# Performance work log

Measured on AMD Instinct MI355X. Metric: run time of the kernel, lower is better.

The kernel has to match this reference:

```python
import jax, jax.numpy as jnp
import numpy as np

E = 1024
H = 16
DH = E // H
LN_EPS = 1e-5


def setup_inputs() -> dict:
    key = jax.random.key(0)
    ks = jax.random.split(key, 9)
    B, Lq, Lk = 8, 1024, 1024
    s = 0.02
    return {
        "query": jax.random.normal(ks[0], (B, Lq, E), jnp.float32),
        "key_t": jax.random.normal(ks[1], (B, Lk, E), jnp.float32),
        "value": jax.random.normal(ks[2], (B, Lk, E), jnp.float32),
        "in_proj_w": jax.random.normal(ks[3], (3 * E, E), jnp.float32) * s,
        "in_proj_b": jnp.zeros((3 * E,), jnp.float32),
        "out_proj_w": jax.random.normal(ks[4], (E, E), jnp.float32) * s,
        "out_proj_b": jnp.zeros((E,), jnp.float32),
        "ln_gamma": jnp.ones((E,), jnp.float32),
        "ln_beta": jnp.zeros((E,), jnp.float32),
    }


def _mha_cross(query, key_t, value, in_proj_w, in_proj_b, out_proj_w, out_proj_b,
               ln_gamma, ln_beta):
    B, Lq, _ = query.shape
    Lk = key_t.shape[1]
    wq, wk, wv = in_proj_w[:E], in_proj_w[E:2 * E], in_proj_w[2 * E:]
    bq, bk, bv = in_proj_b[:E], in_proj_b[E:2 * E], in_proj_b[2 * E:]
    # projections (torch Linear: x @ W^T + b)
    q = (query @ wq.T + bq).reshape(B, Lq, H, DH)
    k = (key_t @ wk.T + bk).reshape(B, Lk, H, DH)
    v = (value @ wv.T + bv).reshape(B, Lk, H, DH)
    scale = 1.0 / np.sqrt(DH).astype(np.float32)
    # unfused attention: explicit [B,H,Lq,Lk] scores (need_weights=True path)
    scores = jnp.einsum("bqhd,bkhd->bhqk", q, k) * scale
    probs = jax.nn.softmax(scores, axis=-1)
    attn = jnp.einsum("bhqk,bkhd->bqhd", probs, v).reshape(B, Lq, E)
    attn_out = attn @ out_proj_w.T + out_proj_b
    # averaged attention weights (average_attn_weights=True default)
    attn_weights = probs.mean(axis=1)  # [B, Lq, Lk]
    # residual + LayerNorm
    x = query + attn_out
    mu = x.mean(axis=-1, keepdims=True)
    var = x.var(axis=-1, keepdims=True)
    y = (x - mu) * jax.lax.rsqrt(var + LN_EPS) * ln_gamma + ln_beta
    return y, attn_weights


def reference(query, key_t, value, in_proj_w, in_proj_b, out_proj_w, out_proj_b,
              ln_gamma, ln_beta):
    return _mha_cross(query, key_t, value, in_proj_w, in_proj_b,
                      out_proj_w, out_proj_b, ln_gamma, ln_beta)
```

## Files before the change

### kernel.cpp

```cpp
#include <hip/hip_runtime.h>
#include <stdint.h>

#define E_DIM 1024
#define H_NUM 16
#define B_NUM 8
#define LQ 1024
#define LK 1024
#define MROWS (B_NUM * LQ)

typedef unsigned short u16;
typedef __attribute__((ext_vector_type(8))) short bf16x8;
typedef __attribute__((ext_vector_type(4))) short bf16x4;
typedef __attribute__((ext_vector_type(4))) float f32x4;
typedef __attribute__((ext_vector_type(2))) unsigned int u32x2;
typedef bf16x8 __attribute__((may_alias)) bf16x8_ma;
typedef bf16x4 __attribute__((may_alias)) bf16x4_ma;
typedef f32x4 __attribute__((may_alias)) f32x4_ma;
typedef u32x2 __attribute__((may_alias)) u32x2_ma;

typedef __attribute__((address_space(1))) const void* gas_ptr;
typedef __attribute__((address_space(3))) void* las_ptr;

__device__ __forceinline__ void gload16(const void* g, void* l) {
  __builtin_amdgcn_global_load_lds((gas_ptr)g, (las_ptr)l, 16, 0, 0);
}

__device__ __forceinline__ u16 f2bf(float f) {
  union { float f; uint32_t u; } c; c.f = f;
  return (u16)((c.u + 0x7FFFu + ((c.u >> 16) & 1u)) >> 16);
}

__device__ __forceinline__ uint32_t pack2bf(float lo, float hi) {
  return __builtin_amdgcn_perm(__float_as_uint(hi), __float_as_uint(lo), 0x07060302u);
}

#define MFMA_BF16(a, b, c) __builtin_amdgcn_mfma_f32_16x16x32_bf16((a), (b), (c), 0, 0, 0)

#define SCALE_Q 0.18033688011112042f


__global__ __launch_bounds__(256) void cvt_f32_bf16(const float* __restrict__ src,
                                                    u16* __restrict__ dst, int n4) {
  int i = blockIdx.x * 256 + threadIdx.x;
  const int stride = gridDim.x * 256;
  for (; i < n4; i += stride) {
    float4 v = ((const float4*)src)[i];
    ushort4 o;
    o.x = f2bf(v.x); o.y = f2bf(v.y); o.z = f2bf(v.z); o.w = f2bf(v.w);
    ((ushort4*)dst)[i] = o;
  }
}

__global__ __launch_bounds__(256) void cvt3_f32_bf16(
    const float* __restrict__ a0, const float* __restrict__ a1, const float* __restrict__ a2,
    u16* __restrict__ o0, u16* __restrict__ o1, u16* __restrict__ o2, int n4) {
  const float* s = (blockIdx.y == 0) ? a0 : (blockIdx.y == 1 ? a1 : a2);
  u16* d = (blockIdx.y == 0) ? o0 : (blockIdx.y == 1 ? o1 : o2);
  int i = blockIdx.x * 256 + threadIdx.x;
  const int stride = gridDim.x * 256;
  for (; i < n4; i += stride) {
    float4 v = ((const float4*)s)[i];
    ushort4 o;
    o.x = f2bf(v.x); o.y = f2bf(v.y); o.z = f2bf(v.z); o.w = f2bf(v.w);
    ((ushort4*)d)[i] = o;
  }
}


#define BAR() __builtin_amdgcn_s_barrier()
#define LGKM0() do { asm volatile("s_waitcnt lgkmcnt(0)" ::: "memory"); \
                     __builtin_amdgcn_sched_barrier(0); } while (0)
#define VMC(n) asm volatile("s_waitcnt vmcnt(" n ")" ::: "memory")

#define ST_A0(t) gload16(pA0 + (size_t)(t) * 32, ldsv + ((t) & 3) * 16384 + wave * 1024)
#define ST_A1(t) gload16(pA1 + (size_t)(t) * 32, ldsv + ((t) & 3) * 16384 + 8192 + wave * 1024)
#define ST_B0(t) gload16(pB0 + (size_t)(t) * 32, ldsv + 65536 + ((t) & 3) * 16384 + wave * 1024)
#define ST_B1(t) gload16(pB1 + (size_t)(t) * 32, ldsv + 65536 + ((t) & 3) * 16384 + 8192 + wave * 1024)

#define RD_A(buf, q)                                                          \
  _Pragma("unroll") for (int jj = 0; jj < 2; ++jj) {                          \
    const int rg = 4 * (q) + 2 * jj + wm;                                     \
    const int rh = (rg & 7) * 16 + lr;                                        \
    afr[jj] = *(const bf16x8_ma*)(ldsc + (buf) * 16384 + ((rg >> 3) << 13) +  \
                                  rh * 64 + rchunk);                          \
  }
#define RD_B(buf)                                                             \
  _Pragma("unroll") for (int n = 0; n < 4; ++n) {                             \
    const int rg = wn4 + n;                                                   \
    const int rh = (rg & 7) * 16 + lr;                                        \
    bfr[n] = *(const bf16x8_ma*)(ldsc + 65536 + (buf) * 16384 +               \
                                 ((rg >> 3) << 13) + rh * 64 + rchunk);       \
  }
#define MMA32(q)                                                              \
  __builtin_amdgcn_s_setprio(1);                                              \
  _Pragma("unroll") for (int jj = 0; jj < 2; ++jj)                            \
    _Pragma("unroll") for (int n = 0; n < 4; ++n)                             \
      acc[2 * (q) + jj][n] = MFMA_BF16(afr[jj], bfr[n], acc[2 * (q) + jj][n]);\
  __builtin_amdgcn_s_setprio(0);

__global__ __launch_bounds__(512, 2) void gemm_qkv(
    const u16* __restrict__ A0, const u16* __restrict__ A1, const u16* __restrict__ A2,
    const u16* __restrict__ W, const float* __restrict__ bias,
    u16* __restrict__ outb, int nwg_n, int nwg_m) {
  __shared__ u16 lds[65536];

  const int tid = threadIdx.x;
  const int wave = tid >> 6, lane = tid & 63;
  const int lr = lane & 15, lg = lane >> 4;
  const int wm = wave >> 2, wn4 = (wave & 3) * 4;

  const int cpx = (int)gridDim.x >> 3;
  const int bid = blockIdx.x;
  const int wg = (bid & 7) * cpx + (bid >> 3);
  const int n_i = wg % nwg_n;
  const int rest = wg / nwg_n;
  const int m_i = rest % nwg_m;
  const int z = rest / nwg_m;
  const int m0 = m_i * 256, n0 = n_i * 256;

  const u16* Az = (z == 0) ? A0 : (z == 1 ? A1 : A2);
  const u16* Wz = W + (size_t)z * E_DIM * E_DIM;
  const float* bs = bias + z * E_DIM;
  const float scale = (z == 0) ? SCALE_Q : 1.0f;

  const int grow = tid >> 2;
  const int gcol = ((tid & 3) ^ ((tid >> 2) & 3) ^ ((tid >> 4) & 3)) * 8;
  const u16* pA0 = Az + (size_t)(m0 + grow) * E_DIM + gcol;
  const u16* pA1 = Az + (size_t)(m0 + 128 + grow) * E_DIM + gcol;
  const u16* pB0 = Wz + (size_t)(n0 + grow) * E_DIM + gcol;
  const u16* pB1 = Wz + (size_t)(n0 + 128 + grow) * E_DIM + gcol;
  char* ldsv = (char*)lds;
  const char* ldsc = (const char*)lds;
  const int rchunk = ((lg ^ (lr & 3) ^ ((lr >> 2) & 3)) << 4);

  const f32x4 fzero = {0.f, 0.f, 0.f, 0.f};
  f32x4 acc[8][4];
#pragma unroll
  for (int j = 0; j < 8; ++j)
#pragma unroll
    for (int n = 0; n < 4; ++n) acc[j][n] = fzero;

#pragma unroll
  for (int t = 0; t < 3; ++t) { ST_A0(t); ST_A1(t); ST_B0(t); ST_B1(t); }
  VMC("8");
  BAR();

  bf16x8 afr[2], bfr[4];
#pragma unroll 1
  for (int i = 0; i < 16; ++i) {
    const int r0 = (2 * i) & 3, r1 = (2 * i + 1) & 3;
    const int ts0 = 2 * i + 3, ts1 = 2 * i + 4;
    const bool s0 = (i <= 14), s1 = (i <= 13);
    RD_B(r0) RD_A(r0, 0)
    if (s0) ST_A0(ts0);
    BAR(); LGKM0();
    MMA32(0)
    BAR();
    RD_A(r0, 1)
    if (s0) ST_A1(ts0);
    BAR(); LGKM0();
    MMA32(1)
    BAR();
    RD_A(r0, 2)
    if (s0) ST_B0(ts0);
    BAR(); LGKM0();
    MMA32(2)
    BAR();
    RD_A(r0, 3)
    if (s0) ST_B1(ts0);
    BAR(); LGKM0();
    MMA32(3)
    if (i <= 14) { VMC("8"); } else { VMC("0"); }
    BAR();
    RD_B(r1) RD_A(r1, 0)
    if (s1) ST_A0(ts1);
    BAR(); LGKM0();
    MMA32(0)
    BAR();
    RD_A(r1, 1)
    if (s1) ST_A1(ts1);
    BAR(); LGKM0();
    MMA32(1)
    BAR();
    RD_A(r1, 2)
    if (s1) ST_B0(ts1);
    BAR(); LGKM0();
    MMA32(2)
    BAR();
    RD_A(r1, 3)
    if (s1) ST_B1(ts1);
    BAR(); LGKM0();
    MMA32(3)
    if (i <= 13) { VMC("8"); } else if (i == 14) { VMC("4"); }
    BAR();
  }

  float bvv[4];
#pragma unroll
  for (int n = 0; n < 4; ++n) bvv[n] = bs[n0 + wn4 * 16 + n * 16 + lr];

  u16* Cb = outb + (size_t)z * (size_t)MROWS * E_DIM;
#pragma unroll
  for (int j = 0; j < 8; ++j) {
    const int rbase = m0 + (2 * j + wm) * 16 + lg * 4;
#pragma unroll
    for (int ii = 0; ii < 4; ++ii) {
      const size_t m = (size_t)(rbase + ii);
#pragma unroll
      for (int n = 0; n < 4; ++n) {
        const int nn = n0 + wn4 * 16 + n * 16 + lr;
        Cb[m * E_DIM + nn] = f2bf((acc[j][n][ii] + bvv[n]) * scale);
      }
    }
  }
}

__global__ __launch_bounds__(256) void gemm128_out(
    const u16* __restrict__ A, const u16* __restrict__ W,
    const float* __restrict__ bias, const float* __restrict__ resid,
    float* __restrict__ outf, int nwg_n, int nwg_m) {
  __shared__ u16 As[128 * 64];
  __shared__ u16 Bs[128 * 64];

  const int tid = threadIdx.x;
  const int wave = tid >> 6;
  const int lane = tid & 63;
  const int lr = lane & 15, lg = lane >> 4;
  const int wr = wave >> 1, wc = wave & 1;

  const int cpx = (int)gridDim.x >> 3;
  const int bid = blockIdx.x;
  const int wg = (bid & 7) * cpx + (bid >> 3);
  const int n_i = wg % nwg_n;
  const int m_i = (wg / nwg_n) % nwg_m;

  const int m0 = m_i * 128;
  const int n0 = n_i * 128;

  const f32x4 fzero = {0.f, 0.f, 0.f, 0.f};
  f32x4 acc[4][4];
#pragma unroll
  for (int a = 0; a < 4; ++a)
#pragma unroll
    for (int b = 0; b < 4; ++b) acc[a][b] = fzero;

  const int lrow8 = lane >> 3;
  const int lcol8 = (lane & 7) * 8;

  for (int kt = 0; kt < E_DIM; kt += 64) {
#pragma unroll
    for (int i = 0; i < 4; ++i) {
      const int seg = i * 4 + wave;
      gload16(W + (size_t)(n0 + seg * 8 + lrow8) * E_DIM + kt + lcol8, &Bs[seg * 512]);
      gload16(A + (size_t)(m0 + seg * 8 + lrow8) * E_DIM + kt + lcol8, &As[seg * 512]);
    }
    __syncthreads();

#pragma unroll
    for (int kk = 0; kk < 64; kk += 32) {
      bf16x8 av[4], bv[4];
#pragma unroll
      for (int t = 0; t < 4; ++t)
        av[t] = *(const bf16x8*)&As[(wr * 64 + t * 16 + lr) * 64 + kk + lg * 8];
#pragma unroll
      for (int t = 0; t < 4; ++t)
        bv[t] = *(const bf16x8*)&Bs[(wc * 64 + t * 16 + lr) * 64 + kk + lg * 8];
#pragma unroll
      for (int mi = 0; mi < 4; ++mi)
#pragma unroll
        for (int ni = 0; ni < 4; ++ni)
          acc[mi][ni] = MFMA_BF16(av[mi], bv[ni], acc[mi][ni]);
    }
    __syncthreads();
  }

  float bvv[4];
#pragma unroll
  for (int ni = 0; ni < 4; ++ni) bvv[ni] = bias[n0 + wc * 64 + ni * 16 + lr];

#pragma unroll
  for (int mi = 0; mi < 4; ++mi) {
#pragma unroll
    for (int i = 0; i < 4; ++i) {
      const size_t m = (size_t)(m0 + wr * 64 + mi * 16 + lg * 4 + i);
#pragma unroll
      for (int ni = 0; ni < 4; ++ni) {
        const int n = n0 + wc * 64 + ni * 16 + lr;
        outf[m * E_DIM + n] = acc[mi][ni][i] + bvv[ni] + resid[m * E_DIM + n];
      }
    }
  }
}

__global__ __launch_bounds__(256) void transpose_v(const u16* __restrict__ Vb,
                                                   u16* __restrict__ Vtg) {
  __shared__ u16 T[64 * 264];
  const int tid = threadIdx.x;
  const int b = blockIdx.z, h = blockIdx.y;
  const int k0 = blockIdx.x * 256;
  const int bh = b * H_NUM + h;
  const int krow = tid >> 3;
  const int d0 = (tid & 7) * 8;
  const int jst = krow & 7;
#pragma unroll
  for (int it = 0; it < 8; ++it) {
    const int k = it * 32 + krow;
    bf16x8 v = *(const bf16x8*)&Vb[(size_t)(b * LK + k0 + k) * E_DIM + h * 64 + d0];
#pragma unroll
    for (int jj = 0; jj < 8; ++jj) {
      const int j = (jj + jst) & 7;
      T[(d0 + j) * 264 + k] = (u16)v[j];
    }
  }
  __syncthreads();
  const int d = tid >> 2;
  const int kk0 = (tid & 3) * 64;
  u16* orow = &Vtg[(size_t)(bh * 64 + d) * LK + k0 + kk0];
#pragma unroll
  for (int c = 0; c < 8; ++c)
    *(bf16x8*)&orow[c * 8] = *(const bf16x8*)&T[d * 264 + kk0 + c * 8];
}

__global__ __launch_bounds__(512) void attn_fwd(
    const u16* __restrict__ Qb, const u16* __restrict__ Kb, const u16* __restrict__ Vtg,
    u16* __restrict__ attnb, float* __restrict__ rden) {
  __shared__ u16 Ks[64 * 72];
  __shared__ u16 Vt[64 * 72];
  __shared__ u16 Pw[8][16 * 72];

  const int tid = threadIdx.x;
  const int wave = tid >> 6, lane = tid & 63;
  const int lr = lane & 15, lg = lane >> 4;

  const int bid = blockIdx.x;
  const int wg = (bid & 7) * 128 + (bid >> 3);
  const int qt = wg & 7;
  const int h = (wg >> 3) & 15;
  const int b = wg >> 7;
  const int bh = b * H_NUM + h;
  const int q0 = qt * 128;

  const size_t qoff = (size_t)(b * LQ + q0 + wave * 16 + lr) * E_DIM + h * 64;
  const bf16x8 qf0 = *(const bf16x8*)&Qb[qoff + lg * 8];
  const bf16x8 qf1 = *(const bf16x8*)&Qb[qoff + 32 + lg * 8];

  const f32x4 fzero = {0.f, 0.f, 0.f, 0.f};
  f32x4 ctx[4];
#pragma unroll
  for (int d = 0; d < 4; ++d) ctx[d] = fzero;
  float dnl = 0.f;

  const int sr = tid >> 3;
  const int sc = (tid & 7) * 8;
  const u16* Kg = &Kb[(size_t)(b * LK + sr) * E_DIM + h * 64 + sc];
  const u16* Vg = &Vtg[(size_t)(bh * 64 + sr) * LK + sc];

  bf16x8 kr = *(const bf16x8*)(Kg);
  bf16x8 vr = *(const bf16x8*)(Vg);
  *(bf16x8*)&Ks[sr * 72 + sc] = kr;
  *(bf16x8*)&Vt[sr * 72 + sc] = vr;

  for (int t = 0; t < 16; ++t) {
    __syncthreads();
    if (t < 15) {
      const int k1 = (t + 1) * 64;
      kr = *(const bf16x8*)(Kg + (size_t)k1 * E_DIM);
      vr = *(const bf16x8*)(Vg + k1);
    }
#pragma unroll
    for (int kf = 0; kf < 4; ++kf) {
      const bf16x8 kb0 = *(const bf16x8*)&Ks[(kf * 16 + lr) * 72 + lg * 8];
      const bf16x8 kb1 = *(const bf16x8*)&Ks[(kf * 16 + lr) * 72 + 32 + lg * 8];
      f32x4 s = fzero;
      s = MFMA_BF16(kb0, qf0, s);
      s = MFMA_BF16(kb1, qf1, s);
      const float p0 = exp2f(s[0]), p1 = exp2f(s[1]);
      const float p2 = exp2f(s[2]), p3 = exp2f(s[3]);
      dnl += (p0 + p1) + (p2 + p3);
      u32x2 w;
      w[0] = pack2bf(p0, p1);
      w[1] = pack2bf(p2, p3);
      *(u32x2_ma*)&Pw[wave][lr * 72 + kf * 16 + lg * 4] = w;
    }
    const bf16x8 pa0 = *(const bf16x8_ma*)&Pw[wave][lr * 72 + lg * 8];
    const bf16x8 pa1 = *(const bf16x8_ma*)&Pw[wave][lr * 72 + 32 + lg * 8];
#pragma unroll
    for (int df = 0; df < 4; ++df) {
      const bf16x8 vb0 = *(const bf16x8*)&Vt[(df * 16 + lr) * 72 + lg * 8];
      const bf16x8 vb1 = *(const bf16x8*)&Vt[(df * 16 + lr) * 72 + 32 + lg * 8];
      ctx[df] = MFMA_BF16(pa0, vb0, ctx[df]);
      ctx[df] = MFMA_BF16(pa1, vb1, ctx[df]);
    }
    __syncthreads();
    if (t < 15) {
      *(bf16x8*)&Ks[sr * 72 + sc] = kr;
      *(bf16x8*)&Vt[sr * 72 + sc] = vr;
    }
  }

  dnl += __shfl_xor(dnl, 16, 64);
  dnl += __shfl_xor(dnl, 32, 64);
  if (lane < 16) rden[(size_t)bh * LQ + q0 + wave * 16 + lane] = 0.0625f / dnl;
  float dnv[4];
#pragma unroll
  for (int i = 0; i < 4; ++i) dnv[i] = __shfl(dnl, lg * 4 + i, 64);

#pragma unroll
  for (int i = 0; i < 4; ++i) {
    const float inv = 1.0f / dnv[i];
    const int q = q0 + wave * 16 + lg * 4 + i;
    const size_t orow = (size_t)(b * LQ + q) * E_DIM + h * 64;
#pragma unroll
    for (int df = 0; df < 4; ++df)
      attnb[orow + df * 16 + lr] = f2bf(ctx[df][i] * inv);
  }
}

__global__ __launch_bounds__(256, 2) void attn_wts(
    const u16* __restrict__ Qb, const u16* __restrict__ Kb,
    const float* __restrict__ rden, float* __restrict__ aw) {
  __shared__ u16 Ks2[2][128 * 72];
  __shared__ u16 Qs[128 * 72];

  const int tid = threadIdx.x;
  const int wave = tid >> 6, lane = tid & 63;
  const int lr = lane & 15, lg = lane >> 4;
  const int wq = wave >> 1, wk = wave & 1;

  const int bid = blockIdx.x;
  const int wg = (bid & 7) * 64 + (bid >> 3);
  const int q0 = (wg & 7) * 128;
  const int k0 = ((wg >> 3) & 7) * 128;
  const int b = wg >> 6;

  const f32x4 fzero = {0.f, 0.f, 0.f, 0.f};
  f32x4 acc[4][4];
#pragma unroll
  for (int t = 0; t < 4; ++t)
#pragma unroll
    for (int j = 0; j < 4; ++j) acc[t][j] = fzero;

  const int sr = tid >> 1;
  const int sc = (tid & 1) * 32;
  const u16* Kg = &Kb[(size_t)(b * LK + k0 + sr) * E_DIM + sc];
  const u16* Qg = &Qb[(size_t)(b * LQ + q0 + sr) * E_DIM + sc];
  const float* dg = &rden[(size_t)(b * H_NUM) * LQ + q0 + wq * 64 + lr];

  bf16x8 kr[4], qr[4];
#pragma unroll
  for (int c = 0; c < 4; ++c) kr[c] = *(const bf16x8*)(Kg + c * 8);
#pragma unroll
  for (int c = 0; c < 4; ++c) qr[c] = *(const bf16x8*)(Qg + c * 8);
#pragma unroll
  for (int c = 0; c < 4; ++c) *(bf16x8*)&Ks2[0][sr * 72 + sc + c * 8] = kr[c];

  for (int h = 0; h < H_NUM; ++h) {
    __syncthreads();
#pragma unroll
    for (int c = 0; c < 4; ++c) *(bf16x8*)&Qs[sr * 72 + sc + c * 8] = qr[c];
    __syncthreads();

    if (h < 15) {
#pragma unroll
      for (int c = 0; c < 4; ++c) kr[c] = *(const bf16x8*)(Kg + (h + 1) * 64 + c * 8);
#pragma unroll
      for (int c = 0; c < 4; ++c) qr[c] = *(const bf16x8*)(Qg + (h + 1) * 64 + c * 8);
    }
    float rd[4];
#pragma unroll
    for (int j = 0; j < 4; ++j) rd[j] = dg[(size_t)h * LQ + j * 16];

    const u16* Kbuf = &Ks2[h & 1][0];
    bf16x8 kb[4][2];
#pragma unroll
    for (int t = 0; t < 4; ++t) {
      const int row = wk * 64 + t * 16 + lr;
      kb[t][0] = *(const bf16x8*)&Kbuf[row * 72 + lg * 8];
      kb[t][1] = *(const bf16x8*)&Kbuf[row * 72 + 32 + lg * 8];
    }
#pragma unroll
    for (int j = 0; j < 4; ++j) {
      const int qrow = wq * 64 + j * 16 + lr;
      const bf16x8 qf0 = *(const bf16x8*)&Qs[qrow * 72 + lg * 8];
      const bf16x8 qf1 = *(const bf16x8*)&Qs[qrow * 72 + 32 + lg * 8];
#pragma unroll
      for (int t = 0; t < 4; ++t) {
        f32x4 s = fzero;
        s = MFMA_BF16(kb[t][0], qf0, s);
        s = MFMA_BF16(kb[t][1], qf1, s);
#pragma unroll
        for (int i = 0; i < 4; ++i)
          acc[t][j][i] += exp2f(s[i]) * rd[j];
      }
    }

    if (h < 15) {
      u16* Kw = &Ks2[(h + 1) & 1][0];
#pragma unroll
      for (int c = 0; c < 4; ++c) *(bf16x8*)&Kw[sr * 72 + sc + c * 8] = kr[c];
    }
  }

#pragma unroll
  for (int j = 0; j < 4; ++j) {
    const size_t orow = (size_t)(b * LQ + q0 + wq * 64 + j * 16 + lr) * LK;
#pragma unroll
    for (int t = 0; t < 4; ++t)
      *(f32x4_ma*)&aw[orow + k0 + wk * 64 + t * 16 + lg * 4] = acc[t][j];
  }
}

__global__ __launch_bounds__(256) void ln_kernel(float* __restrict__ xy,
                                                 const float* __restrict__ gamma,
                                                 const float* __restrict__ beta) {
  __shared__ float ls[4], ls2[4];
  const int row = blockIdx.x;
  const int tid = threadIdx.x;
  float4* xr = (float4*)(xy + (size_t)row * E_DIM);
  float4 v = xr[tid];
  float s = v.x + v.y + v.z + v.w;
  float s2 = v.x * v.x + v.y * v.y + v.z * v.z + v.w * v.w;
#pragma unroll
  for (int off = 32; off >= 1; off >>= 1) {
    s += __shfl_xor(s, off, 64);
    s2 += __shfl_xor(s2, off, 64);
  }
  const int wave = tid >> 6, lane = tid & 63;
  if (lane == 0) { ls[wave] = s; ls2[wave] = s2; }
  __syncthreads();
  s = ls[0] + ls[1] + ls[2] + ls[3];
  s2 = ls2[0] + ls2[1] + ls2[2] + ls2[3];
  const float mu = s * (1.0f / E_DIM);
  const float var = s2 * (1.0f / E_DIM) - mu * mu;
  const float rs = rsqrtf(var + 1e-5f);
  const float4 g = ((const float4*)gamma)[tid];
  const float4 bt = ((const float4*)beta)[tid];
  float4 o;
  o.x = (v.x - mu) * rs * g.x + bt.x;
  o.y = (v.y - mu) * rs * g.y + bt.y;
  o.z = (v.z - mu) * rs * g.z + bt.z;
  o.w = (v.w - mu) * rs * g.w + bt.w;
  xr[tid] = o;
}

extern "C" void kernel_launch(void* const* d_in, const int* in_sizes, int n_in,
                              void* d_out, int out_size, void* d_ws, size_t ws_size,
                              hipStream_t stream) {
  (void)in_sizes; (void)n_in; (void)out_size; (void)ws_size;
  const float* query     = (const float*)d_in[0];
  const float* key_t     = (const float*)d_in[1];
  const float* value     = (const float*)d_in[2];
  const float* in_proj_b = (const float*)d_in[4];
  const float* out_proj_b = (const float*)d_in[6];
  const float* ln_gamma  = (const float*)d_in[7];
  const float* ln_beta   = (const float*)d_in[8];

  float* y  = (float*)d_out;
  float* aw = y + (size_t)B_NUM * LQ * E_DIM;

  const size_t SZ = (size_t)B_NUM * LQ * E_DIM;
  u16* ws    = (u16*)d_ws;
  u16* Qb    = ws;
  u16* Kb    = ws + SZ;
  u16* Vb    = ws + 2 * SZ;
  u16* attnb = ws + 3 * SZ;
  u16* wqkvb = ws + 4 * SZ;
  u16* woutb = wqkvb + 3 * E_DIM * E_DIM;
  float* rden = (float*)(wqkvb + 4 * (size_t)E_DIM * E_DIM);

  u16* Xq  = (u16*)aw;
  u16* Xk  = Xq + SZ;
  u16* Xv  = (u16*)y;
  u16* Vtg = (u16*)y;

  cvt_f32_bf16<<<3072, 256, 0, stream>>>((const float*)d_in[3], wqkvb, (3 * E_DIM * E_DIM) / 4);
  cvt_f32_bf16<<<1024, 256, 0, stream>>>((const float*)d_in[5], woutb, (E_DIM * E_DIM) / 4);
  cvt3_f32_bf16<<<dim3(2048, 3), 256, 0, stream>>>(query, key_t, value, Xq, Xk, Xv, (int)(SZ / 4));

  gemm_qkv<<<384, 512, 0, stream>>>(
      Xq, Xk, Xv, wqkvb, in_proj_b, Qb, 4, 32);

  transpose_v<<<dim3(4, 16, 8), 256, 0, stream>>>(Vb, Vtg);

  attn_fwd<<<1024, 512, 0, stream>>>(Qb, Kb, Vtg, attnb, rden);

  attn_wts<<<512, 256, 0, stream>>>(Qb, Kb, rden, aw);

  gemm128_out<<<512, 256, 0, stream>>>(attnb, woutb, out_proj_b, query, y, 8, 64);

  ln_kernel<<<8192, 256, 0, stream>>>(y, ln_gamma, ln_beta);
}
```

Baseline: 269.2 us.

## Simplify QKV GEMM to double-buffered LDS pipeline with fewer barriers

Replaces the 4-stage LDS ring with fine-grained per-quarter barriers and priority hints in the QKV projection GEMM by a plain two-buffer scheme. Each K-step loads all A/B fragments at once and issues all 32 MFMAs. LDS halves to 64KB and launch bounds ask for 4 workgroups per CU. The XOR swizzle on LDS chunk placement is removed, which may add bank conflicts. The shallower prefetch depth may expose global-load latency, and 4 blocks of 512 threads with large accumulators may not fit in registers.

```diff
diff --git a/kernel.cpp b/kernel.cpp
--- a/kernel.cpp
+++ b/kernel.cpp
@@ -67,42 +67,37 @@
 }
 
 
-#define BAR() __builtin_amdgcn_s_barrier()
-#define LGKM0() do { asm volatile("s_waitcnt lgkmcnt(0)" ::: "memory"); \
-                     __builtin_amdgcn_sched_barrier(0); } while (0)
-#define VMC(n) asm volatile("s_waitcnt vmcnt(" n ")" ::: "memory")
-
-#define ST_A0(t) gload16(pA0 + (size_t)(t) * 32, ldsv + ((t) & 3) * 16384 + wave * 1024)
-#define ST_A1(t) gload16(pA1 + (size_t)(t) * 32, ldsv + ((t) & 3) * 16384 + 8192 + wave * 1024)
-#define ST_B0(t) gload16(pB0 + (size_t)(t) * 32, ldsv + 65536 + ((t) & 3) * 16384 + wave * 1024)
-#define ST_B1(t) gload16(pB1 + (size_t)(t) * 32, ldsv + 65536 + ((t) & 3) * 16384 + 8192 + wave * 1024)
-
-#define RD_A(buf, q)                                                          \
-  _Pragma("unroll") for (int jj = 0; jj < 2; ++jj) {                          \
-    const int rg = 4 * (q) + 2 * jj + wm;                                     \
-    const int rh = (rg & 7) * 16 + lr;                                        \
-    afr[jj] = *(const bf16x8_ma*)(ldsc + (buf) * 16384 + ((rg >> 3) << 13) +  \
-                                  rh * 64 + rchunk);                          \
-  }
-#define RD_B(buf)                                                             \
-  _Pragma("unroll") for (int n = 0; n < 4; ++n) {                             \
-    const int rg = wn4 + n;                                                   \
-    const int rh = (rg & 7) * 16 + lr;                                        \
-    bfr[n] = *(const bf16x8_ma*)(ldsc + 65536 + (buf) * 16384 +               \
-                                 ((rg >> 3) << 13) + rh * 64 + rchunk);       \
-  }
-#define MMA32(q)                                                              \
-  __builtin_amdgcn_s_setprio(1);                                              \
-  _Pragma("unroll") for (int jj = 0; jj < 2; ++jj)                            \
-    _Pragma("unroll") for (int n = 0; n < 4; ++n)                             \
-      acc[2 * (q) + jj][n] = MFMA_BF16(afr[jj], bfr[n], acc[2 * (q) + jj][n]);\
-  __builtin_amdgcn_s_setprio(0);
-
-__global__ __launch_bounds__(512, 2) void gemm_qkv(
+#define STG(t, buf) do {                                                     \
+    const size_t kc = (size_t)(t) * 32;                                      \
+    gload16(pA0 + kc, ldsv + (buf) * 16384 + segoff);                        \
+    gload16(pA1 + kc, ldsv + (buf) * 16384 + 8192 + segoff);                 \
+    gload16(pB0 + kc, ldsv + 32768 + (buf) * 16384 + segoff);                \
+    gload16(pB1 + kc, ldsv + 32768 + (buf) * 16384 + 8192 + segoff);         \
+  } while (0)
+
+#define RDQ(buf)                                                             \
+  _Pragma("unroll") for (int j = 0; j < 8; ++j) {                            \
+    const int rga = 2 * j + wm;                                              \
+    av[j] = *(const bf16x8_ma*)(ldsc + (buf) * 16384 + ((rga >> 3) << 13) +  \
+                                ((rga & 7) << 10) + lr * 64 + lg * 16);      \
+  }                                                                          \
+  _Pragma("unroll") for (int n = 0; n < 4; ++n) {                            \
+    const int rgb = wn4 + n;                                                 \
+    bv[n] = *(const bf16x8_ma*)(ldsc + 32768 + (buf) * 16384 +               \
+                                ((rgb >> 3) << 13) + ((rgb & 7) << 10) +     \
+                                lr * 64 + lg * 16);                          \
+  }
+
+#define MMAQ()                                                               \
+  _Pragma("unroll") for (int j = 0; j < 8; ++j)                              \
+    _Pragma("unroll") for (int n = 0; n < 4; ++n)                            \
+      acc[j][n] = MFMA_BF16(av[j], bv[n], acc[j][n]);
+
+__global__ __launch_bounds__(512, 4) void gemm_qkv(
     const u16* __restrict__ A0, const u16* __restrict__ A1, const u16* __restrict__ A2,
     const u16* __restrict__ W, const float* __restrict__ bias,
     u16* __restrict__ outb, int nwg_n, int nwg_m) {
-  __shared__ u16 lds[65536];
+  __shared__ u16 lds[32768];
 
   const int tid = threadIdx.x;
   const int wave = tid >> 6, lane = tid & 63;
@@ -124,14 +119,14 @@
   const float scale = (z == 0) ? SCALE_Q : 1.0f;
 
   const int grow = tid >> 2;
-  const int gcol = ((tid & 3) ^ ((tid >> 2) & 3) ^ ((tid >> 4) & 3)) * 8;
+  const int gcol = (tid & 3) * 8;
   const u16* pA0 = Az + (size_t)(m0 + grow) * E_DIM + gcol;
   const u16* pA1 = Az + (size_t)(m0 + 128 + grow) * E_DIM + gcol;
   const u16* pB0 = Wz + (size_t)(n0 + grow) * E_DIM + gcol;
   const u16* pB1 = Wz + (size_t)(n0 + 128 + grow) * E_DIM + gcol;
   char* ldsv = (char*)lds;
   const char* ldsc = (const char*)lds;
-  const int rchunk = ((lg ^ (lr & 3) ^ ((lr >> 2) & 3)) << 4);
+  const int segoff = tid * 16;
 
   const f32x4 fzero = {0.f, 0.f, 0.f, 0.f};
   f32x4 acc[8][4];
@@ -140,59 +135,21 @@
 #pragma unroll
     for (int n = 0; n < 4; ++n) acc[j][n] = fzero;
 
-#pragma unroll
-  for (int t = 0; t < 3; ++t) { ST_A0(t); ST_A1(t); ST_B0(t); ST_B1(t); }
-  VMC("8");
-  BAR();
-
-  bf16x8 afr[2], bfr[4];
+  bf16x8 av[8], bv[4];
+
+  STG(0, 0);
+  __syncthreads();
+
 #pragma unroll 1
-  for (int i = 0; i < 16; ++i) {
-    const int r0 = (2 * i) & 3, r1 = (2 * i + 1) & 3;
-    const int ts0 = 2 * i + 3, ts1 = 2 * i + 4;
-    const bool s0 = (i <= 14), s1 = (i <= 13);
-    RD_B(r0) RD_A(r0, 0)
-    if (s0) ST_A0(ts0);
-    BAR(); LGKM0();
-    MMA32(0)
-    BAR();
-    RD_A(r0, 1)
-    if (s0) ST_A1(ts0);
-    BAR(); LGKM0();
-    MMA32(1)
-    BAR();
-    RD_A(r0, 2)
-    if (s0) ST_B0(ts0);
-    BAR(); LGKM0();
-    MMA32(2)
-    BAR();
-    RD_A(r0, 3)
-    if (s0) ST_B1(ts0);
-    BAR(); LGKM0();
-    MMA32(3)
-    if (i <= 14) { VMC("8"); } else { VMC("0"); }
-    BAR();
-    RD_B(r1) RD_A(r1, 0)
-    if (s1) ST_A0(ts1);
-    BAR(); LGKM0();
-    MMA32(0)
-    BAR();
-    RD_A(r1, 1)
-    if (s1) ST_A1(ts1);
-    BAR(); LGKM0();
-    MMA32(1)
-    BAR();
-    RD_A(r1, 2)
-    if (s1) ST_B0(ts1);
-    BAR(); LGKM0();
-    MMA32(2)
-    BAR();
-    RD_A(r1, 3)
-    if (s1) ST_B1(ts1);
-    BAR(); LGKM0();
-    MMA32(3)
-    if (i <= 13) { VMC("8"); } else if (i == 14) { VMC("4"); }
-    BAR();
+  for (int t = 0; t < 32; t += 2) {
+    STG(t + 1, 1);
+    RDQ(0)
+    MMAQ()
+    __syncthreads();
+    if (t < 30) STG(t + 2, 0);
+    RDQ(1)
+    MMAQ()
+    __syncthreads();
   }
 
   float bvv[4];
```

New measurement: 670.8 us. 149% more time.
